# Kernel tuning notes

Measured on AMD Instinct MI355X. Metric: run time of the kernel, lower is better.

## Reference

```python
import jax, jax.numpy as jnp
import numpy as np
from jax import lax

B, C, N, T, K = 16, 64, 512, 64, 3
EPS = 1e-5


def _bn(x, g, b):
    # training-mode BatchNorm2d over (B, H=N, W=T) per channel
    m = jnp.mean(x, axis=(0, 2, 3), keepdims=True)
    v = jnp.var(x, axis=(0, 2, 3), keepdims=True)
    return (x - m) * lax.rsqrt(v + EPS) * g[None, :, None, None] + b[None, :, None, None]


def _conv(x, w, b, pad):
    y = lax.conv_general_dilated(x, w, (1, 1), ((0, 0), pad),
                                 dimension_numbers=('NCHW', 'OIHW', 'NCHW'))
    return y + b[None, :, None, None]


def setup_inputs() -> dict:
    key = jax.random.key(0)
    ks = jax.random.split(key, 8)
    xav = lambda k, sh, fi, fo: jax.random.normal(k, sh, jnp.float32) * np.sqrt(2.0 / (fi + fo))
    return {
        'x': jax.random.normal(ks[0], (B, C, N, T), jnp.float32),
        'adj_mx': jax.random.normal(ks[1], (K, N, N), jnp.float32) / np.sqrt(N),
        'cheb_w': xav(ks[2], (K, C, C), C, C),
        'cheb_b': jnp.zeros((C,), jnp.float32),
        'w1': xav(ks[3], (C, C, 1, 3), 3 * C, 3 * C),
        'b1': jnp.zeros((C,), jnp.float32),
        'g1': jnp.ones((C,), jnp.float32),
        'be1': jnp.zeros((C,), jnp.float32),
        'w2': xav(ks[4], (C, C, 1, 3), 3 * C, 3 * C),
        'b2': jnp.zeros((C,), jnp.float32),
        'g2': jnp.ones((C,), jnp.float32),
        'be2': jnp.zeros((C,), jnp.float32),
        'gate_w': xav(ks[5], (C, 2 * C, 1, 1), 2 * C, C),
        'gate_b': jnp.zeros((C,), jnp.float32),
        'res_w': xav(ks[6], (C, C, 1, 1), C, C),
        'res_b': jnp.zeros((C,), jnp.float32),
        'g3': jnp.ones((C,), jnp.float32),
        'be3': jnp.zeros((C,), jnp.float32),
    }


def _forward(x, adj_mx, cheb_w, cheb_b, w1, b1, g1, be1, w2, b2, g2, be2,
             gate_w, gate_b, res_w, res_b, g3, be3):
    # ChebFilterBlock: out[b,o,n,t] = sum_{k,i,m} x[b,i,m,t] adj[k,m,n] W[k,i,o] + bias
    spatial = jnp.einsum('bimt,kmn,kio->bont', x, adj_mx, cheb_w) \
              + cheb_b[None, :, None, None]
    # temporal branch: two (1,3) convs with BN+ReLU
    t = jax.nn.relu(_bn(_conv(x, w1, b1, (1, 1)), g1, be1))
    t = jax.nn.relu(_bn(_conv(t, w2, b2, (1, 1)), g2, be2))
    # gated fusion
    comb = jnp.concatenate([spatial, t], axis=1)
    gate = jax.nn.sigmoid(_conv(comb, gate_w, gate_b, (0, 0)))
    res = _conv(x, res_w, res_b, (0, 0))
    out = gate * spatial + (1.0 - gate) * t + res
    return _bn(out, g3, be3)


def reference(x, adj_mx, cheb_w, cheb_b, w1, b1, g1, be1, w2, b2, g2, be2,
              gate_w, gate_b, res_w, res_b, g3, be3):
    return _forward(x, adj_mx, cheb_w, cheb_b, w1, b1, g1, be1, w2, b2, g2, be2,
                    gate_w, gate_b, res_w, res_b, g3, be3)
```

## Files before the change

kernel.cpp:

```cpp
#include <hip/hip_runtime.h>
#include <hip/hip_bf16.h>
#include <cstdint>

#define BB 16
#define CC 64
#define NN 512
#define TT 64
#define KCH 3
#define PP (BB*NN*TT)
#define EPSB 1e-5f

typedef __bf16 bf16;
typedef __bf16 bf16x8 __attribute__((ext_vector_type(8)));
typedef __bf16 bf16x4 __attribute__((ext_vector_type(4)));
typedef float  f32x4  __attribute__((ext_vector_type(4)));

#define MFMA16(A,Bv,Cv) __builtin_amdgcn_mfma_f32_16x16x32_bf16((A),(Bv),(Cv),0,0,0)

__device__ __forceinline__ void gload_lds16(const bf16* g, bf16* l){
  __builtin_amdgcn_global_load_lds(
      (const __attribute__((address_space(1))) void*)g,
      (__attribute__((address_space(3))) void*)l, 16, 0, 0);
}

__global__ __launch_bounds__(256) void k_adjT(const float* __restrict__ adj,
                                              bf16* __restrict__ adjb){
  int idx = blockIdx.x*256 + threadIdx.x;
  int m = idx & 511, n = (idx >> 9) & 511, k = idx >> 18;
  adjb[idx] = (bf16)adj[((size_t)(k*512 + m))*512 + n];
}

__global__ __launch_bounds__(256) void k_wprep(const float* __restrict__ w1,
    const float* __restrict__ w2, const float* __restrict__ cw,
    const float* __restrict__ gw, const float* __restrict__ rw,
    bf16* __restrict__ w1p, bf16* __restrict__ w2p, bf16* __restrict__ cp,
    bf16* __restrict__ gp, bf16* __restrict__ rp){
  int tid = threadIdx.x;
  for (int e = tid; e < 6*2048; e += 256){
    int j = e&7, lane = (e>>3)&63, cf = (e>>9)&3, ks = e>>11;
    int k = ks*32 + (lane>>4)*8 + j, col = cf*16 + (lane&15);
    int kk = k >> 6, i = k & 63;
    w1p[e] = (bf16)w1[(col*64 + i)*3 + kk];
    w2p[e] = (bf16)w2[(col*64 + i)*3 + kk];
    cp[e]  = (bf16)cw[((size_t)kk*64 + i)*64 + col];
  }
  for (int e = tid; e < 4*2048; e += 256){
    int j = e&7, lane = (e>>3)&63, cf = (e>>9)&3, ks = e>>11;
    int k = ks*32 + (lane>>4)*8 + j, col = cf*16 + (lane&15);
    gp[e] = (bf16)gw[col*128 + k];
  }
  for (int e = tid; e < 2*2048; e += 256){
    int j = e&7, lane = (e>>3)&63, cf = (e>>9)&3, ks = e>>11;
    int k = ks*32 + (lane>>4)*8 + j, col = cf*16 + (lane&15);
    rp[e] = (bf16)rw[col*64 + k];
  }
}

__global__ __launch_bounds__(256) void k_xlb(const float* __restrict__ x,
                                             bf16* __restrict__ xlb){
  __shared__ float tile[64][65];
  int bn = blockIdx.x; int b = bn >> 9, n = bn & 511;
  int tid = threadIdx.x;
  const float* xp = x + ((size_t)(b*64)*512 + n)*64;
  for (int p = 0; p < 4; ++p){
    int q = p*256 + tid;
    int i = q >> 4, tc = (q & 15)*4;
    float4 v = *reinterpret_cast<const float4*>(xp + (size_t)i*512*64 + tc);
    tile[i][tc+0] = v.x; tile[i][tc+1] = v.y; tile[i][tc+2] = v.z; tile[i][tc+3] = v.w;
  }
  __syncthreads();
  bf16* op = xlb + (size_t)bn*4096;
  for (int p = 0; p < 2; ++p){
    int v8 = p*256 + tid;
    int t = v8 >> 3, ic = (v8 & 7)*8;
    bf16x8 o;
    #pragma unroll
    for (int e = 0; e < 8; ++e) o[e] = (bf16)tile[ic+e][t];
    *reinterpret_cast<bf16x8*>(op + t*64 + ic) = o;
  }
}

__global__ __launch_bounds__(256) void k_xmt(const float* __restrict__ x,
                                             bf16* __restrict__ xmt){
  __shared__ bf16 lds[16][16][72];
  int bid = blockIdx.x;
  int t0 = (bid & 3)*16, m0 = ((bid>>2)&7)*64, i0 = ((bid>>5)&3)*16, b = bid>>7;
  int tid = threadIdx.x;
  int tq = tid & 3, m = tid >> 2;
  for (int i = 0; i < 16; ++i){
    float4 v = *reinterpret_cast<const float4*>(
        x + ((size_t)(b*64 + i0 + i)*512 + (m0 + m))*64 + t0 + tq*4);
    lds[tq*4+0][i][m] = (bf16)v.x; lds[tq*4+1][i][m] = (bf16)v.y;
    lds[tq*4+2][i][m] = (bf16)v.z; lds[tq*4+3][i][m] = (bf16)v.w;
  }
  __syncthreads();
  for (int p = 0; p < 8; ++p){
    int row = p*32 + (tid >> 3); int t = row >> 4, i = row & 15, mc = tid & 7;
    bf16x8 v = *reinterpret_cast<const bf16x8*>(&lds[t][i][mc*8]);
    *reinterpret_cast<bf16x8*>(
        xmt + ((size_t)((b*64 + t0 + t)*64) + i0 + i)*512 + m0 + mc*8) = v;
  }
}

__global__ __launch_bounds__(256,4) void k_conv(const bf16* __restrict__ in,
    const bf16* __restrict__ wp, bf16* __restrict__ outp, float* __restrict__ part,
    const float* __restrict__ sc, const float* __restrict__ sh){
  int tid = threadIdx.x, w = tid >> 6, l = tid & 63, l15 = l & 15, lg = l >> 4;
  int blk = blockIdx.x;
  size_t rowbase = (size_t)blk * 64;
  const bf16* xr = in + rowbase * 64;
  int t = w*16 + l15;
  f32x4 acc[4] = {};
  #pragma unroll
  for (int ks = 0; ks < 6; ++ks){
    int dt = ks >> 1, kh = ks & 1;
    int ts = t + dt - 1;
    bf16x8 a = {};
    if (ts >= 0 && ts < 64){
      a = *reinterpret_cast<const bf16x8*>(xr + ts*64 + kh*32 + lg*8);
      if (sc){
        int i0 = kh*32 + lg*8;
        #pragma unroll
        for (int e = 0; e < 8; ++e){
          float f = (float)a[e]*sc[i0+e] + sh[i0+e];
          a[e] = (bf16)fmaxf(f, 0.f);
        }
      }
    }
    #pragma unroll
    for (int cf = 0; cf < 4; ++cf){
      bf16x8 bfr = *reinterpret_cast<const bf16x8*>(wp + ((ks*4 + cf)*64 + l)*8);
      acc[cf] = MFMA16(a, bfr, acc[cf]);
    }
  }
  __shared__ float ssum[4][4][16], ssq[4][4][16];
  #pragma unroll
  for (int cf = 0; cf < 4; ++cf){
    int o = cf*16 + l15;
    float s = 0.f, q = 0.f;
    #pragma unroll
    for (int r = 0; r < 4; ++r){
      float vv = acc[cf][r];
      int to = w*16 + lg*4 + r;
      outp[(rowbase + to)*64 + o] = (bf16)vv;
      s += vv; q += vv*vv;
    }
    s += __shfl_xor(s, 16); s += __shfl_xor(s, 32);
    q += __shfl_xor(q, 16); q += __shfl_xor(q, 32);
    if (lg == 0){ ssum[w][cf][l15] = s; ssq[w][cf][l15] = q; }
  }
  __syncthreads();
  if (tid < 64){
    int cf = tid >> 4, c = tid & 15;
    float s = ssum[0][cf][c]+ssum[1][cf][c]+ssum[2][cf][c]+ssum[3][cf][c];
    float q = ssq[0][cf][c]+ssq[1][cf][c]+ssq[2][cf][c]+ssq[3][cf][c];
    part[(size_t)blk*128 + tid*2]     = s;
    part[(size_t)blk*128 + tid*2 + 1] = q;
  }
}

__global__ __launch_bounds__(256) void k_stats(const float* __restrict__ part, int nb,
    const float* __restrict__ g, const float* __restrict__ be,
    float* __restrict__ sc, float* __restrict__ sh){
  int c = blockIdx.x, tid = threadIdx.x;
  float s = 0.f, q = 0.f;
  for (int i = tid; i < nb; i += 256){
    s += part[(size_t)i*128 + c*2];
    q += part[(size_t)i*128 + c*2 + 1];
  }
  __shared__ float rs[256], rq[256];
  rs[tid] = s; rq[tid] = q; __syncthreads();
  for (int st = 128; st > 0; st >>= 1){
    if (tid < st){ rs[tid] += rs[tid+st]; rq[tid] += rq[tid+st]; }
    __syncthreads();
  }
  if (tid == 0){
    float cnt = (float)PP;
    float mean = rs[0]/cnt, var = rq[0]/cnt - mean*mean;
    float r = rsqrtf(var + EPSB);
    sc[c] = g[c]*r;
    sh[c] = be[c] - mean*g[c]*r;
  }
}

__global__ __launch_bounds__(256,2) void k_gemm1(const bf16* __restrict__ xmt,
    const bf16* __restrict__ adjb, const bf16* __restrict__ cp,
    const float* __restrict__ cb, bf16* __restrict__ spm){
  __shared__ bf16 As[2][128*32];
  __shared__ bf16 Bs[2][128*32];
  __shared__ bf16 VT[128*128];

  int tid = threadIdx.x, w = tid >> 6, l = tid & 63, l15 = l & 15, lg = l >> 4;
  int wr = w >> 1, wc = w & 1;

  int orig = blockIdx.x;
  int wg = (orig & 7) * 256 + (orig >> 3);
  int jt = wg >> 2, nt = wg & 3;
  int J0 = jt*128, N0 = nt*128;

  const bf16* aglob = xmt + (size_t)J0*512;

  auto stage = [&](int buf, int m0, const bf16* bg){
    #pragma unroll
    for (int p = 0; p < 2; ++p){
      int idx = p*256 + tid;
      int r = idx >> 2, c = idx & 3;
      int cg = c ^ (r & 3);
      gload_lds16(aglob + (size_t)r*512 + m0 + cg*8,
                  &As[buf][(p*256 + w*64)*8]);
      gload_lds16(bg + (size_t)r*512 + m0 + cg*8,
                  &Bs[buf][(p*256 + w*64)*8]);
    }
  };

  f32x4 acc2[4][4] = {};
  const bf16* bglob = adjb + (size_t)N0*512;
  stage(0, 0, bglob);
  __syncthreads();

  int buf = 0;
  int tw = w >> 1;
  for (int kk = 0; kk < 3; ++kk){
    f32x4 acc[4][4] = {};
    for (int ks = 0; ks < 16; ++ks){
      if (ks < 15) stage(buf ^ 1, (ks+1)*32, bglob);
      bf16x8 a[4], bb[4];
      #pragma unroll
      for (int rf = 0; rf < 4; ++rf){
        int row = wr*64 + rf*16 + l15;
        a[rf] = *reinterpret_cast<const bf16x8*>(
            &As[buf][row*32 + ((lg ^ (row & 3))*8)]);
      }
      #pragma unroll
      for (int cf = 0; cf < 4; ++cf){
        int row = wc*64 + cf*16 + l15;
        bb[cf] = *reinterpret_cast<const bf16x8*>(
            &Bs[buf][row*32 + ((lg ^ (row & 3))*8)]);
      }
      #pragma unroll
      for (int rf = 0; rf < 4; ++rf)
        #pragma unroll
        for (int cf = 0; cf < 4; ++cf)
          acc[rf][cf] = MFMA16(a[rf], bb[cf], acc[rf][cf]);
      __syncthreads();
      buf ^= 1;
    }

    #pragma unroll
    for (int rf = 0; rf < 4; ++rf){
      int jb = wr*8 + rf*2 + (lg >> 1);
      #pragma unroll
      for (int cf = 0; cf < 4; ++cf){
        int n = wc*64 + cf*16 + l15;
        bf16x4 pk;
        #pragma unroll
        for (int r = 0; r < 4; ++r) pk[r] = (bf16)acc[rf][cf][r];
        *reinterpret_cast<bf16x4*>(
            &VT[n*128 + ((jb ^ (n & 15)) << 3) + ((lg & 1) << 2)]) = pk;
      }
    }
    if (kk < 2){
      bglob = adjb + ((size_t)(kk+1)*512 + N0)*512;
      stage(buf, 0, bglob);
    }
    __syncthreads();

    #pragma unroll
    for (int ks2 = 0; ks2 < 2; ++ks2){
      bf16x8 bc[4];
      #pragma unroll
      for (int cf = 0; cf < 4; ++cf)
        bc[cf] = *reinterpret_cast<const bf16x8*>(
            cp + (((kk*2 + ks2)*4 + cf)*64 + l)*8);
      #pragma unroll
      for (int rf = 0; rf < 4; ++rf){
        int n = (w & 1)*64 + rf*16 + l15;
        int jb = tw*8 + ks2*4 + lg;
        bf16x8 a2 = *reinterpret_cast<const bf16x8*>(
            &VT[n*128 + ((jb ^ (n & 15)) << 3)]);
        #pragma unroll
        for (int cf = 0; cf < 4; ++cf)
          acc2[rf][cf] = MFMA16(a2, bc[cf], acc2[rf][cf]);
      }
    }
    __syncthreads();
  }

  bf16* SP = VT;
  float cbv[4];
  #pragma unroll
  for (int cf = 0; cf < 4; ++cf) cbv[cf] = cb[cf*16 + l15];
  #pragma unroll
  for (int rf = 0; rf < 4; ++rf){
    int rowb = w*64 + rf*16 + lg*4;
    #pragma unroll
    for (int cf = 0; cf < 4; ++cf){
      int o = cf*16 + l15;
      #pragma unroll
      for (int r = 0; r < 4; ++r)
        SP[(rowb + r)*64 + o] = (bf16)(acc2[rf][cf][r] + cbv[cf]);
    }
  }
  __syncthreads();
  int b = jt >> 5, t0 = (jt & 31)*2;
  #pragma unroll
  for (int q = 0; q < 8; ++q){
    int flat = q*256 + tid;
    int row = flat >> 3, oc = (flat & 7)*8;
    int tl = row >> 7, n = N0 + (row & 127);
    bf16x8 vv = *reinterpret_cast<const bf16x8*>(&SP[row*64 + oc]);
    *reinterpret_cast<bf16x8*>(
        &spm[(((size_t)b*512 + n)*64 + (t0 + tl))*64 + oc]) = vv;
  }
}

__global__ __launch_bounds__(256,4) void k_fusion(const bf16* __restrict__ spm,
    const bf16* __restrict__ t2, const bf16* __restrict__ xlb,
    const bf16* __restrict__ gp, const bf16* __restrict__ rp,
    const float* __restrict__ sc2, const float* __restrict__ sh2,
    const float* __restrict__ gateb, bf16* __restrict__ pre,
    float* __restrict__ part){
  int tid = threadIdx.x, w = tid >> 6, l = tid & 63, l15 = l & 15, lg = l >> 4;
  int blk = blockIdx.x;
  int b = blk >> 9, n = blk & 511;
  size_t rowbase = (size_t)blk * 64;
  int t = w*16 + l15;
  f32x4 ag[4] = {}, ar[4] = {};
  #pragma unroll
  for (int ks = 0; ks < 4; ++ks){
    bf16x8 a;
    if (ks < 2){
      a = *reinterpret_cast<const bf16x8*>(spm + (rowbase + t)*64 + ks*32 + lg*8);
    } else {
      int i0 = (ks-2)*32 + lg*8;
      bf16x8 raw = *reinterpret_cast<const bf16x8*>(t2 + (rowbase + t)*64 + i0);
      #pragma unroll
      for (int e = 0; e < 8; ++e){
        float f = (float)raw[e]*sc2[i0+e] + sh2[i0+e];
        a[e] = (bf16)fmaxf(f, 0.f);
      }
    }
    #pragma unroll
    for (int cf = 0; cf < 4; ++cf){
      bf16x8 bfr = *reinterpret_cast<const bf16x8*>(gp + ((ks*4 + cf)*64 + l)*8);
      ag[cf] = MFMA16(a, bfr, ag[cf]);
    }
  }
  #pragma unroll
  for (int ks = 0; ks < 2; ++ks){
    bf16x8 a = *reinterpret_cast<const bf16x8*>(xlb + (rowbase + t)*64 + ks*32 + lg*8);
    #pragma unroll
    for (int cf = 0; cf < 4; ++cf){
      bf16x8 bfr = *reinterpret_cast<const bf16x8*>(rp + ((ks*4 + cf)*64 + l)*8);
      ar[cf] = MFMA16(a, bfr, ar[cf]);
    }
  }
  __shared__ float ssum[4][4][16], ssq[4][4][16];
  int tb = w*16 + lg*4;
  #pragma unroll
  for (int cf = 0; cf < 4; ++cf){
    int o = cf*16 + l15;
    float gb = gateb[o], sco = sc2[o], sho = sh2[o];
    float s = 0.f, q = 0.f;
    bf16x4 ov;
    #pragma unroll
    for (int r = 0; r < 4; ++r){
      size_t row = rowbase + tb + r;
      float z = ag[cf][r] + gb;
      float g = 1.f/(1.f + __expf(-z));
      float spv = (float)spm[row*64 + o];
      float tv  = (float)t2[row*64 + o];
      tv = fmaxf(tv*sco + sho, 0.f);
      float val = g*spv + (1.f - g)*tv + ar[cf][r];
      ov[r] = (bf16)val;
      s += val; q += val*val;
    }
    *reinterpret_cast<bf16x4*>(pre + (((size_t)b*64 + o)*512 + n)*64 + tb) = ov;
    s += __shfl_xor(s, 16); s += __shfl_xor(s, 32);
    q += __shfl_xor(q, 16); q += __shfl_xor(q, 32);
    if (lg == 0){ ssum[w][cf][l15] = s; ssq[w][cf][l15] = q; }
  }
  __syncthreads();
  if (tid < 64){
    int cf = tid >> 4, c = tid & 15;
    float s = ssum[0][cf][c]+ssum[1][cf][c]+ssum[2][cf][c]+ssum[3][cf][c];
    float q = ssq[0][cf][c]+ssq[1][cf][c]+ssq[2][cf][c]+ssq[3][cf][c];
    part[(size_t)blk*128 + tid*2]     = s;
    part[(size_t)blk*128 + tid*2 + 1] = q;
  }
}

__global__ __launch_bounds__(256) void k_bn3(const bf16* __restrict__ pre,
    float* __restrict__ out,
    const float* __restrict__ sc, const float* __restrict__ sh){
  size_t total8 = (size_t)BB*CC*NN*TT/8;
  for (size_t i8 = (size_t)blockIdx.x*256 + threadIdx.x; i8 < total8;
       i8 += (size_t)gridDim.x*256){
    bf16x8 v = reinterpret_cast<const bf16x8*>(pre)[i8];
    int o = (int)(i8 >> 12) & 63;
    float a = sc[o], bsh = sh[o];
    float4 r0, r1;
    r0.x = (float)v[0]*a + bsh; r0.y = (float)v[1]*a + bsh;
    r0.z = (float)v[2]*a + bsh; r0.w = (float)v[3]*a + bsh;
    r1.x = (float)v[4]*a + bsh; r1.y = (float)v[5]*a + bsh;
    r1.z = (float)v[6]*a + bsh; r1.w = (float)v[7]*a + bsh;
    reinterpret_cast<float4*>(out)[i8*2]     = r0;
    reinterpret_cast<float4*>(out)[i8*2 + 1] = r1;
  }
}

extern "C" void kernel_launch(void* const* d_in, const int* in_sizes, int n_in,
                              void* d_out, int out_size, void* d_ws, size_t ws_size,
                              hipStream_t stream){
  (void)in_sizes; (void)n_in; (void)out_size; (void)ws_size;
  const float* x   = (const float*)d_in[0];
  const float* adj = (const float*)d_in[1];
  const float* cw  = (const float*)d_in[2];
  const float* cb  = (const float*)d_in[3];
  const float* w1  = (const float*)d_in[4];
  const float* g1  = (const float*)d_in[6];
  const float* be1 = (const float*)d_in[7];
  const float* w2  = (const float*)d_in[8];
  const float* g2  = (const float*)d_in[10];
  const float* be2 = (const float*)d_in[11];
  const float* gw  = (const float*)d_in[12];
  const float* gb  = (const float*)d_in[13];
  const float* rw  = (const float*)d_in[14];
  const float* g3  = (const float*)d_in[16];
  const float* be3 = (const float*)d_in[17];
  float* out = (float*)d_out;

  char* ws = (char*)d_ws;
  size_t off = 0;
  auto alloc = [&](size_t bytes)->char*{
    char* p = ws + off; off += (bytes + 255) & ~(size_t)255; return p;
  };
  bf16* xlb  = (bf16*)alloc((size_t)PP*64*2);
  bf16* xmt  = (bf16*)alloc((size_t)PP*64*2);
  bf16* t1   = (bf16*)alloc((size_t)PP*64*2);
  bf16* t2   = (bf16*)alloc((size_t)PP*64*2);
  bf16* spm  = t1;
  bf16* pre  = xmt;
  bf16* adjb = (bf16*)alloc((size_t)KCH*512*512*2);
  bf16* w1p  = (bf16*)alloc(6*2048*2);
  bf16* w2p  = (bf16*)alloc(6*2048*2);
  bf16* cp   = (bf16*)alloc(6*2048*2);
  bf16* gp   = (bf16*)alloc(4*2048*2);
  bf16* rp   = (bf16*)alloc(2*2048*2);
  float* part = (float*)alloc((size_t)8192*128*4);
  float* s1sc = (float*)alloc(256); float* s1sh = (float*)alloc(256);
  float* s2sc = (float*)alloc(256); float* s2sh = (float*)alloc(256);
  float* s3sc = (float*)alloc(256); float* s3sh = (float*)alloc(256);

  k_adjT <<<dim3(3072), dim3(256), 0, stream>>>(adj, adjb);
  k_wprep<<<dim3(1),    dim3(256), 0, stream>>>(w1, w2, cw, gw, rw, w1p, w2p, cp, gp, rp);
  k_xlb  <<<dim3(8192), dim3(256), 0, stream>>>(x, xlb);
  k_xmt  <<<dim3(2048), dim3(256), 0, stream>>>(x, xmt);

  k_conv <<<dim3(8192), dim3(256), 0, stream>>>(xlb, w1p, t1, part, nullptr, nullptr);
  k_stats<<<dim3(64),   dim3(256), 0, stream>>>(part, 8192, g1, be1, s1sc, s1sh);
  k_conv <<<dim3(8192), dim3(256), 0, stream>>>(t1, w2p, t2, part, s1sc, s1sh);
  k_stats<<<dim3(64),   dim3(256), 0, stream>>>(part, 8192, g2, be2, s2sc, s2sh);

  k_gemm1<<<dim3(2048), dim3(256), 0, stream>>>(xmt, adjb, cp, cb, spm);

  k_fusion<<<dim3(8192), dim3(256), 0, stream>>>(spm, t2, xlb, gp, rp,
                                                 s2sc, s2sh, gb, pre, part);
  k_stats<<<dim3(64),   dim3(256), 0, stream>>>(part, 8192, g3, be3, s3sc, s3sh);
  k_bn3  <<<dim3(2048), dim3(256), 0, stream>>>(pre, out, s3sc, s3sh);
}
```

Before: 624.0 us.

## Triple-buffer GEMM1 LDS staging with explicit vmcnt waits for deeper prefetch

Moves the k_gemm1 main loop from double-buffered to triple-buffered LDS staging, prefetching two K-steps ahead. Blanket __syncthreads are replaced with explicit s_waitcnt vmcnt/lgkmcnt counts and raw s_barrier, so global-to-LDS loads can stay in flight across iterations. This is meant to hide global load latency behind the MFMA work. In exchange it uses more LDS, which may limit occupancy at 2 blocks per CU, and the hand-counted waitcnts are fragile if the number of loads changes.

```diff
diff --git a/kernel.cpp b/kernel.cpp
--- a/kernel.cpp
+++ b/kernel.cpp
@@ -186,8 +186,8 @@
 __global__ __launch_bounds__(256,2) void k_gemm1(const bf16* __restrict__ xmt,
     const bf16* __restrict__ adjb, const bf16* __restrict__ cp,
     const float* __restrict__ cb, bf16* __restrict__ spm){
-  __shared__ bf16 As[2][128*32];
-  __shared__ bf16 Bs[2][128*32];
+  __shared__ bf16 As[3][128*32];
+  __shared__ bf16 Bs[3][128*32];
   __shared__ bf16 VT[128*128];
 
   int tid = threadIdx.x, w = tid >> 6, l = tid & 63, l15 = l & 15, lg = l >> 4;
@@ -216,34 +216,42 @@
   f32x4 acc2[4][4] = {};
   const bf16* bglob = adjb + (size_t)N0*512;
   stage(0, 0, bglob);
-  __syncthreads();
-
-  int buf = 0;
+  stage(1, 32, bglob);
+
   int tw = w >> 1;
   for (int kk = 0; kk < 3; ++kk){
     f32x4 acc[4][4] = {};
     for (int ks = 0; ks < 16; ++ks){
-      if (ks < 15) stage(buf ^ 1, (ks+1)*32, bglob);
+      if (ks <= 13) stage((ks+2)%3, (ks+2)*32, bglob);
+      if (ks <= 13)      asm volatile("s_waitcnt vmcnt(8)" ::: "memory");
+      else if (ks == 14) asm volatile("s_waitcnt vmcnt(4)" ::: "memory");
+      else               asm volatile("s_waitcnt vmcnt(0)" ::: "memory");
+      __builtin_amdgcn_s_barrier();
+      __builtin_amdgcn_sched_barrier(0);
+
+      int cbuf = ks % 3;
       bf16x8 a[4], bb[4];
       #pragma unroll
       for (int rf = 0; rf < 4; ++rf){
         int row = wr*64 + rf*16 + l15;
         a[rf] = *reinterpret_cast<const bf16x8*>(
-            &As[buf][row*32 + ((lg ^ (row & 3))*8)]);
+            &As[cbuf][row*32 + ((lg ^ (row & 3))*8)]);
       }
       #pragma unroll
       for (int cf = 0; cf < 4; ++cf){
         int row = wc*64 + cf*16 + l15;
         bb[cf] = *reinterpret_cast<const bf16x8*>(
-            &Bs[buf][row*32 + ((lg ^ (row & 3))*8)]);
+            &Bs[cbuf][row*32 + ((lg ^ (row & 3))*8)]);
       }
       #pragma unroll
       for (int rf = 0; rf < 4; ++rf)
         #pragma unroll
         for (int cf = 0; cf < 4; ++cf)
           acc[rf][cf] = MFMA16(a[rf], bb[cf], acc[rf][cf]);
-      __syncthreads();
-      buf ^= 1;
+
+      asm volatile("s_waitcnt lgkmcnt(0)" ::: "memory");
+      __builtin_amdgcn_sched_barrier(0);
+      __builtin_amdgcn_s_barrier();
     }
 
     #pragma unroll
@@ -261,9 +269,12 @@
     }
     if (kk < 2){
       bglob = adjb + ((size_t)(kk+1)*512 + N0)*512;
-      stage(buf, 0, bglob);
-    }
-    __syncthreads();
+      stage(0, 0, bglob);
+      stage(1, 32, bglob);
+    }
+    asm volatile("s_waitcnt lgkmcnt(0)" ::: "memory");
+    __builtin_amdgcn_sched_barrier(0);
+    __builtin_amdgcn_s_barrier();
 
     #pragma unroll
     for (int ks2 = 0; ks2 < 2; ++ks2){
@@ -283,7 +294,9 @@
           acc2[rf][cf] = MFMA16(a2, bc[cf], acc2[rf][cf]);
       }
     }
-    __syncthreads();
+    asm volatile("s_waitcnt lgkmcnt(0)" ::: "memory");
+    __builtin_amdgcn_sched_barrier(0);
+    __builtin_amdgcn_s_barrier();
   }
 
   bf16* SP = VT;
```

Result: no change. 623.0 us (-0.2%).
